# Kernel optimization log

Hardware: AMD Instinct MI355X
Metric: run time of the kernel (lower is better)

## Reference

```python
import jax, jax.numpy as jnp
import numpy as np

J = 1.0          # coupling constant
PT_PERIOD = 4    # parallel-tempering exchange every PT_PERIOD sweeps


def setup_inputs() -> dict:
    key = jax.random.key(0)
    k1, k2 = jax.random.split(key)
    B, C, L = 32, 16, 256
    # temperatures across the Ising critical region, sorted ascending
    T = jnp.sort(1.5 + 2.0 * jax.random.uniform(k1, (B,), dtype=jnp.float32))
    # spins stored as {0,1} ints; converted to +/-1 inside reference
    spins = jax.random.randint(k2, (B, C, L, L), 0, 2).astype(jnp.int32)
    return {"T": T, "spins": spins, "n_sweeps": 16}


def _neighbor_sum(s):
    # periodic 4-neighbor sum, shape preserved [B,C,L,L]
    return (jnp.roll(s, 1, -1) + jnp.roll(s, -1, -1)
            + jnp.roll(s, 1, -2) + jnp.roll(s, -1, -2))


def _energy(s):
    # total Ising energy per chain: -J * sum_<ij> s_i s_j  -> [B, C]
    return -J * jnp.sum(s * (jnp.roll(s, -1, -1) + jnp.roll(s, -1, -2)), axis=(-1, -2))


def reference(T, spins, n_sweeps):
    B, C, L, _ = spins.shape
    s = spins.astype(jnp.float32) * 2.0 - 1.0          # +/-1 spins
    ii = jnp.arange(L)
    parity = (ii[:, None] + ii[None, :]) % 2            # [L,L] checkerboard
    Tb = T[:, None, None, None]                         # [B,1,1,1]
    beta = 1.0 / T                                      # [B]
    base_key = jax.random.key(42)

    def half_sweep(s, key, color):
        dE = 2.0 * J * s * _neighbor_sum(s)             # local energy change on flip
        u = jax.random.uniform(key, s.shape, dtype=jnp.float32)
        acc = u < jnp.exp(-dE / Tb)                     # Metropolis accept
        mask = (parity == color)                        # update one sub-lattice only
        return jnp.where(mask & acc, -s, s)

    def pt_swap(s, key, pair_parity):
        # attempt swaps between adjacent temperatures (b, b+1) with given pair parity
        E = _energy(s)                                  # [B, C]
        d = (beta[:-1] - beta[1:])[:, None] * (E[:-1] - E[1:])   # [B-1, C]
        u = jax.random.uniform(key, (B - 1, C), dtype=jnp.float32)
        pair_mask = (jnp.arange(B - 1) % 2) == pair_parity
        acc = (u < jnp.exp(d)) & pair_mask[:, None]     # [B-1, C] non-overlapping
        swap_next = jnp.concatenate([acc, jnp.zeros((1, C), bool)], 0)  # swap b<->b+1
        swap_prev = jnp.concatenate([jnp.zeros((1, C), bool), acc], 0)
        s_next = jnp.roll(s, -1, axis=0)
        s_prev = jnp.roll(s, 1, axis=0)
        swn = swap_next[:, :, None, None]
        swp = swap_prev[:, :, None, None]
        return jnp.where(swn, s_next, jnp.where(swp, s_prev, s))

    def sweep(s, t):
        kb = jax.random.fold_in(base_key, t)
        k1, k2, k3 = jax.random.split(kb, 3)
        s = half_sweep(s, k1, 0)   # black sub-lattice
        s = half_sweep(s, k2, 1)   # white sub-lattice
        do_pt = (t % PT_PERIOD) == (PT_PERIOD - 1)
        s = jax.lax.cond(do_pt,
                         lambda s_: pt_swap(s_, k3, (t // PT_PERIOD) % 2),
                         lambda s_: s_, s)
        return s, None

    s, _ = jax.lax.scan(sweep, s, jnp.arange(n_sweeps))
    return s, _energy(s)
```

## Files before the change

### kernel.cpp

```cpp
#include <hip/hip_runtime.h>
#include <stdint.h>


#define BB 32
#define CC 16
#define PLANE 65536
#define NSITE (BB * CC * PLANE)
#define NPAIR ((BB - 1) * CC)

__host__ __device__ __forceinline__ void tf2x32(uint32_t k0, uint32_t k1,
                                                uint32_t c0, uint32_t c1,
                                                uint32_t& o0, uint32_t& o1) {
  uint32_t ks2 = k0 ^ k1 ^ 0x1BD11BDAu;
  uint32_t x0 = c0 + k0;
  uint32_t x1 = c1 + k1;
#define TF_ROT(r) { x0 += x1; x1 = (x1 << (r)) | (x1 >> (32 - (r))); x1 ^= x0; }
  TF_ROT(13) TF_ROT(15) TF_ROT(26) TF_ROT(6)
  x0 += k1;  x1 += ks2 + 1u;
  TF_ROT(17) TF_ROT(29) TF_ROT(16) TF_ROT(24)
  x0 += ks2; x1 += k0 + 2u;
  TF_ROT(13) TF_ROT(15) TF_ROT(26) TF_ROT(6)
  x0 += k0;  x1 += k1 + 3u;
  TF_ROT(17) TF_ROT(29) TF_ROT(16) TF_ROT(24)
  x0 += k1;  x1 += ks2 + 4u;
  TF_ROT(13) TF_ROT(15) TF_ROT(26) TF_ROT(6)
  x0 += ks2; x1 += k0 + 5u;
#undef TF_ROT
  o0 = x0; o1 = x1;
}

__device__ __forceinline__ uint32_t tf_bits(uint32_t k0, uint32_t k1,
                                            uint32_t ks2, uint32_t x1i) {
  uint32_t x0 = k0, x1 = x1i;
#define R4(a,b,c,d) \
  x0 += x1; x1 = __builtin_rotateleft32(x1, (a)); x1 ^= x0; \
  x0 += x1; x1 = __builtin_rotateleft32(x1, (b)); x1 ^= x0; \
  x0 += x1; x1 = __builtin_rotateleft32(x1, (c)); x1 ^= x0; \
  x0 += x1; x1 = __builtin_rotateleft32(x1, (d)); x1 ^= x0;
  R4(13,15,26,6)  x0 += k1;  x1 += ks2 + 1u;
  R4(17,29,16,24) x0 += ks2; x1 += k0 + 2u;
  R4(13,15,26,6)  x0 += k0;  x1 += k1 + 3u;
  R4(17,29,16,24) x0 += k1;  x1 += ks2 + 4u;
  R4(13,15,26,6)  x0 += ks2; x1 += k0 + 5u;
#undef R4
  return x0 ^ x1;
}

__device__ __forceinline__ float u01(uint32_t bits) {
  return __uint_as_float((bits >> 9) | 0x3f800000u) - 1.0f;
}

__global__ __launch_bounds__(256) void init8_k(const int* __restrict__ spins,
                                               uint8_t* __restrict__ s) {
  int i = blockIdx.x * 256 + threadIdx.x;
  int4 v = ((const int4*)spins)[i];
  uint32_t o = ((uint32_t)(uint8_t)(int8_t)(2 * v.x - 1))
             | ((uint32_t)(uint8_t)(int8_t)(2 * v.y - 1) << 8)
             | ((uint32_t)(uint8_t)(int8_t)(2 * v.z - 1) << 16)
             | ((uint32_t)(uint8_t)(int8_t)(2 * v.w - 1) << 24);
  ((uint32_t*)s)[i] = o;
}

__global__ void prep_k(const float* __restrict__ T,
                       uint32_t* __restrict__ M4, uint32_t* __restrict__ M8) {
  int b = threadIdx.x;
  if (b < BB) {
    float t = T[b];
    float th4 = (float)exp((double)((-4.0f) / t));
    float th8 = (float)exp((double)((-8.0f) / t));
    M4[b] = (uint32_t)ceil((double)th4 * 8388608.0);
    M8[b] = (uint32_t)ceil((double)th8 * 8388608.0);
  }
}

__device__ __forceinline__ void do_color(uint32_t* __restrict__ tile,
    int w, int lane, int lm, int lp, uint32_t vk, int color,
    uint32_t k0, uint32_t k1, uint32_t ks2, uint32_t M4b, uint32_t M8b) {
#pragma unroll 4
  for (int it = 0; it < 16; ++it) {
    int j  = w + it * 16;
    int rb = j << 6;
    int ju = ((j + 255) & 255) << 6;
    int jd = ((j + 1) & 255) << 6;
    int p  = (j + color) & 1;
    uint32_t soff = (uint32_t)((j << 8) + p);

    uint32_t cur = tile[rb + lane];
    uint32_t up  = tile[ju + lane];
    uint32_t dn  = tile[jd + lane];
    uint32_t pw  = tile[rb + lm];
    uint32_t nw  = tile[rb + lp];
    uint32_t lft = __builtin_amdgcn_alignbit(cur, pw, 24);
    uint32_t rgt = __builtin_amdgcn_alignbit(nw, cur, 8);
    uint32_t kd2 = (up & 0x02020202u) + (dn & 0x02020202u)
                 + (lft & 0x02020202u) + (rgt & 0x02020202u);

    uint32_t flip = 0;
    {
      uint32_t kdi = (kd2 >> (8 * p)) & 0xFFu;
      uint32_t si  = (cur >> (8 * p + 1)) & 1u;
      uint32_t m2  = si ? (8u - kdi) : kdi;
      bool a = true;
      if (m2 < 4u) {
        uint32_t n = tf_bits(k0, k1, ks2, vk + soff) >> 9;
        a = n < (m2 == 2u ? M4b : M8b);
      }
      if (a) flip |= 0xFEu << (8 * p);
    }
    {
      uint32_t kdi = (kd2 >> (8 * p + 16)) & 0xFFu;
      uint32_t si  = (cur >> (8 * p + 17)) & 1u;
      uint32_t m2  = si ? (8u - kdi) : kdi;
      bool a = true;
      if (m2 < 4u) {
        uint32_t n = tf_bits(k0, k1, ks2, vk + soff + 2u) >> 9;
        a = n < (m2 == 2u ? M4b : M8b);
      }
      if (a) flip |= 0xFE0000u << (8 * p);
    }
    tile[rb + lane] = cur ^ flip;
  }
}

__global__ __launch_bounds__(1024) void sweep4_k(
    uint8_t* __restrict__ sg,
    const uint32_t* __restrict__ M4, const uint32_t* __restrict__ M8,
    uint4 kS0, uint4 kS1, uint4 kS2, uint4 kS3,
    int tbase, const int* __restrict__ nsw, float* __restrict__ Eplane) {
  __shared__ uint32_t tile[16384];
  int tid = threadIdx.x;
  int bc  = blockIdx.x;
  int b   = bc >> 4;
  uint32_t bcbase = (uint32_t)bc << 16;
  uint32_t* gp = (uint32_t*)(sg + ((size_t)bc << 16));
  uint32_t M4b = M4[b], M8b = M8[b];
  int nswv = *nsw;

  for (int i = tid; i < 4096; i += 1024)
    ((uint4*)tile)[i] = ((const uint4*)gp)[i];
  __syncthreads();

  int w    = __builtin_amdgcn_readfirstlane(tid >> 6);
  int lane = tid & 63;
  int lm   = (lane + 63) & 63, lp = (lane + 1) & 63;

  uint4 keys[4] = {kS0, kS1, kS2, kS3};
#pragma unroll
  for (int ss = 0; ss < 4; ++ss) {
    if (tbase + ss < nswv) {
      uint32_t kA0 = keys[ss].x, kA1 = keys[ss].y;
      uint32_t kB0 = keys[ss].z, kB1 = keys[ss].w;
      uint32_t ksA = kA0 ^ kA1 ^ 0x1BD11BDAu;
      uint32_t ksB = kB0 ^ kB1 ^ 0x1BD11BDAu;
      uint32_t vkA = kA1 + bcbase + (uint32_t)(lane << 2);
      uint32_t vkB = kB1 + bcbase + (uint32_t)(lane << 2);
      do_color(tile, w, lane, lm, lp, vkA, 0, kA0, kA1, ksA, M4b, M8b);
      __syncthreads();
      do_color(tile, w, lane, lm, lp, vkB, 1, kB0, kB1, ksB, M4b, M8b);
      __syncthreads();
    }
  }

  int acc = 0;
  for (int it = 0; it < 16; ++it) {
    int j = w + it * 16;
    uint32_t cur = tile[(j << 6) + lane];
    uint32_t nxt = tile[(j << 6) + lp];
    uint32_t dwn = tile[((((j + 1) & 255)) << 6) + lane];
    uint32_t rsh = (cur >> 8) | (nxt << 24);
    int d = __builtin_popcount((cur ^ rsh) & 0x02020202u)
          + __builtin_popcount((cur ^ dwn) & 0x02020202u);
    acc += 8 - 2 * d;
  }

  for (int i = tid; i < 4096; i += 1024)
    ((uint4*)gp)[i] = ((uint4*)tile)[i];
  __syncthreads();

  for (int off = 32; off > 0; off >>= 1) acc += __shfl_down(acc, off, 64);
  if (lane == 0) tile[w] = (uint32_t)acc;
  __syncthreads();
  if (tid == 0) {
    int tot = 0;
    for (int i = 0; i < 16; ++i) tot += (int)tile[i];
    Eplane[bc] = -(float)tot;
  }
}

__global__ void pt_decide_k(const float* __restrict__ Eplane,
                            const float* __restrict__ T,
                            uint32_t k0, uint32_t k1, int pair_parity,
                            int* __restrict__ accf, int t,
                            const int* __restrict__ nsw) {
  int tid = threadIdx.x;
  if (tid >= NPAIR) return;
  if (t >= *nsw) { accf[tid] = 0; return; }
  int b = tid >> 4;
  float d = (1.0f / T[b] - 1.0f / T[b + 1]) * (Eplane[tid] - Eplane[tid + 16]);
  uint32_t h0, h1;
  tf2x32(k0, k1, 0u, (uint32_t)tid, h0, h1);
  float u = u01(h0 ^ h1);
  float th = (float)exp((double)d);
  accf[tid] = (u < th) && ((b & 1) == pair_parity);
}

__global__ __launch_bounds__(256) void pt_swap8_k(uint8_t* __restrict__ s,
                                                  const int* __restrict__ accf) {
  int pc = blockIdx.x;
  if (!accf[pc]) return;
  uint4* p0 = (uint4*)(s + ((size_t)pc << 16));
  uint4* p1 = p0 + (CC * PLANE / 16);
  for (int j = threadIdx.x; j < PLANE / 16; j += 256) {
    uint4 a0 = p0[j], a1 = p1[j];
    p0[j] = a1; p1[j] = a0;
  }
}

__global__ void final_eout_k(const float* __restrict__ Eplane,
                             const int* __restrict__ accf,
                             float* __restrict__ Eout) {
  int tid = threadIdx.x;
  int b = tid >> 4;
  float e = Eplane[tid];
  if (b < 31 && accf[tid])      e = Eplane[tid + 16];
  if (b > 0  && accf[tid - 16]) e = Eplane[tid - 16];
  Eout[tid] = e;
}

__global__ __launch_bounds__(256) void expand_k(const int8_t* __restrict__ st,
                                                float* __restrict__ out,
                                                int lo, int cnt4) {
  int i = blockIdx.x * 256 + threadIdx.x;
  if (i >= cnt4) return;
  uint32_t v = *(const uint32_t*)(st + lo + 4 * i);
  float4 o;
  o.x = (float)(int8_t)(v);
  o.y = (float)(int8_t)(v >> 8);
  o.z = (float)(int8_t)(v >> 16);
  o.w = (float)(int8_t)(v >> 24);
  ((float4*)out)[(lo >> 2) + i] = o;
}

__global__ __launch_bounds__(256) void expand_head_k(const int8_t* __restrict__ st,
                                                     float* __restrict__ out) {
  uint32_t r[8];
  int t = threadIdx.x;
  for (int u = 0; u < 8; ++u) r[u] = *(const uint32_t*)(st + t * 32 + 4 * u);
  __syncthreads();
  for (int u = 0; u < 8; ++u) {
    uint32_t v = r[u];
    float4 o;
    o.x = (float)(int8_t)(v);
    o.y = (float)(int8_t)(v >> 8);
    o.z = (float)(int8_t)(v >> 16);
    o.w = (float)(int8_t)(v >> 24);
    ((float4*)out)[t * 8 + u] = o;
  }
}

extern "C" void kernel_launch(void* const* d_in, const int* in_sizes, int n_in,
                              void* d_out, int out_size, void* d_ws, size_t ws_size,
                              hipStream_t stream) {
  (void)in_sizes; (void)n_in; (void)out_size; (void)ws_size;
  const float* T    = (const float*)d_in[0];
  const int*  spins = (const int*)d_in[1];
  const int*  nsw   = (const int*)d_in[2];

  uint8_t* buf0 = (uint8_t*)d_out;
  float*   outf = (float*)d_out;
  float*   Eout = outf + NSITE;

  float*    Eplane = (float*)d_ws;
  uint32_t* M4     = (uint32_t*)(Eplane + 512);
  uint32_t* M8     = M4 + BB;
  int*      accf   = (int*)(M8 + BB);

  init8_k<<<NSITE / 1024, 256, 0, stream>>>(spins, buf0);
  prep_k<<<1, 64, 0, stream>>>(T, M4, M8);

  for (int g = 0; g < 4; ++g) {
    uint4 kS[4];
    uint32_t k3a = 0, k3b = 0;
    for (int i = 0; i < 4; ++i) {
      int t = 4 * g + i;
      uint32_t kb0, kb1;
      tf2x32(0u, 42u, 0u, (uint32_t)t, kb0, kb1);
      tf2x32(kb0, kb1, 0u, 0u, kS[i].x, kS[i].y);
      tf2x32(kb0, kb1, 0u, 1u, kS[i].z, kS[i].w);
      if (i == 3) tf2x32(kb0, kb1, 0u, 2u, k3a, k3b);
    }
    sweep4_k<<<BB * CC, 1024, 0, stream>>>(buf0, M4, M8,
                                           kS[0], kS[1], kS[2], kS[3],
                                           4 * g, nsw, Eplane);
    pt_decide_k<<<1, 512, 0, stream>>>(Eplane, T, k3a, k3b, g & 1,
                                       accf, 4 * g + 3, nsw);
    pt_swap8_k<<<NPAIR, 256, 0, stream>>>(buf0, accf);
  }

  final_eout_k<<<1, 512, 0, stream>>>(Eplane, accf, Eout);

  for (int lo = NSITE / 4; lo >= 8192; lo >>= 2) {
    int cnt4 = (lo * 3) / 4;
    expand_k<<<(cnt4 + 255) / 256, 256, 0, stream>>>((int8_t*)buf0, outf, lo, cnt4);
  }
  expand_head_k<<<1, 256, 0, stream>>>((int8_t*)buf0, outf);
}
```

Before: 1.464 ms.

## Fuse spin init into first sweep kernel and make Metropolis RNG branch-free

Drops the separate init8_k kernel and has the first sweep4_k launch read the int32 spins directly, pack them into int8 in shared memory, and skip one global write-and-read round trip. The Metropolis step now always computes both Threefry draws and picks thresholds with selects, so there is no divergent branch around the RNG. The rotate uses alignbit and the unroll factor drops from 4 to 2. Computing the RNG unconditionally adds ALU work for sites that would have been accepted anyway, in exchange for uniform control flow and less register pressure.

New measurement: 1.731 ms. 1.18x slower.

```diff
diff --git a/kernel.cpp b/kernel.cpp
--- a/kernel.cpp
+++ b/kernel.cpp
@@ -29,36 +29,29 @@
   o0 = x0; o1 = x1;
 }
 
-__device__ __forceinline__ uint32_t tf_bits(uint32_t k0, uint32_t k1,
-                                            uint32_t ks2, uint32_t x1i) {
+__device__ __forceinline__ uint32_t rotl(uint32_t x, int r) {
+  return __builtin_amdgcn_alignbit(x, x, 32 - r);
+}
+
+__device__ __forceinline__ uint32_t tf_bits9(uint32_t k0, uint32_t k1,
+                                             uint32_t ks2, uint32_t x1i) {
   uint32_t x0 = k0, x1 = x1i;
 #define R4(a,b,c,d) \
-  x0 += x1; x1 = __builtin_rotateleft32(x1, (a)); x1 ^= x0; \
-  x0 += x1; x1 = __builtin_rotateleft32(x1, (b)); x1 ^= x0; \
-  x0 += x1; x1 = __builtin_rotateleft32(x1, (c)); x1 ^= x0; \
-  x0 += x1; x1 = __builtin_rotateleft32(x1, (d)); x1 ^= x0;
+  x0 += x1; x1 = rotl(x1, (a)); x1 ^= x0; \
+  x0 += x1; x1 = rotl(x1, (b)); x1 ^= x0; \
+  x0 += x1; x1 = rotl(x1, (c)); x1 ^= x0; \
+  x0 += x1; x1 = rotl(x1, (d)); x1 ^= x0;
   R4(13,15,26,6)  x0 += k1;  x1 += ks2 + 1u;
   R4(17,29,16,24) x0 += ks2; x1 += k0 + 2u;
   R4(13,15,26,6)  x0 += k0;  x1 += k1 + 3u;
   R4(17,29,16,24) x0 += k1;  x1 += ks2 + 4u;
   R4(13,15,26,6)  x0 += ks2; x1 += k0 + 5u;
 #undef R4
-  return x0 ^ x1;
+  return (x0 ^ x1) >> 9;
 }
 
 __device__ __forceinline__ float u01(uint32_t bits) {
   return __uint_as_float((bits >> 9) | 0x3f800000u) - 1.0f;
-}
-
-__global__ __launch_bounds__(256) void init8_k(const int* __restrict__ spins,
-                                               uint8_t* __restrict__ s) {
-  int i = blockIdx.x * 256 + threadIdx.x;
-  int4 v = ((const int4*)spins)[i];
-  uint32_t o = ((uint32_t)(uint8_t)(int8_t)(2 * v.x - 1))
-             | ((uint32_t)(uint8_t)(int8_t)(2 * v.y - 1) << 8)
-             | ((uint32_t)(uint8_t)(int8_t)(2 * v.z - 1) << 16)
-             | ((uint32_t)(uint8_t)(int8_t)(2 * v.w - 1) << 24);
-  ((uint32_t*)s)[i] = o;
 }
 
 __global__ void prep_k(const float* __restrict__ T,
@@ -76,14 +69,14 @@
 __device__ __forceinline__ void do_color(uint32_t* __restrict__ tile,
     int w, int lane, int lm, int lp, uint32_t vk, int color,
     uint32_t k0, uint32_t k1, uint32_t ks2, uint32_t M4b, uint32_t M8b) {
-#pragma unroll 4
+#pragma unroll 2
   for (int it = 0; it < 16; ++it) {
     int j  = w + it * 16;
     int rb = j << 6;
     int ju = ((j + 255) & 255) << 6;
     int jd = ((j + 1) & 255) << 6;
-    int p  = (j + color) & 1;
-    uint32_t soff = (uint32_t)((j << 8) + p);
+    int p8 = ((j + color) & 1) << 3;
+    uint32_t soff = (uint32_t)((j << 8) | (p8 >> 3));
 
     uint32_t cur = tile[rb + lane];
     uint32_t up  = tile[ju + lane];
@@ -95,35 +88,29 @@
     uint32_t kd2 = (up & 0x02020202u) + (dn & 0x02020202u)
                  + (lft & 0x02020202u) + (rgt & 0x02020202u);
 
-    uint32_t flip = 0;
-    {
-      uint32_t kdi = (kd2 >> (8 * p)) & 0xFFu;
-      uint32_t si  = (cur >> (8 * p + 1)) & 1u;
-      uint32_t m2  = si ? (8u - kdi) : kdi;
-      bool a = true;
-      if (m2 < 4u) {
-        uint32_t n = tf_bits(k0, k1, ks2, vk + soff) >> 9;
-        a = n < (m2 == 2u ? M4b : M8b);
-      }
-      if (a) flip |= 0xFEu << (8 * p);
-    }
-    {
-      uint32_t kdi = (kd2 >> (8 * p + 16)) & 0xFFu;
-      uint32_t si  = (cur >> (8 * p + 17)) & 1u;
-      uint32_t m2  = si ? (8u - kdi) : kdi;
-      bool a = true;
-      if (m2 < 4u) {
-        uint32_t n = tf_bits(k0, k1, ks2, vk + soff + 2u) >> 9;
-        a = n < (m2 == 2u ? M4b : M8b);
-      }
-      if (a) flip |= 0xFE0000u << (8 * p);
-    }
+    uint32_t nA = tf_bits9(k0, k1, ks2, vk + soff);
+    uint32_t nB = tf_bits9(k0, k1, ks2, vk + soff + 2u);
+
+    uint32_t kdA = (kd2 >> p8) & 0xFFu;
+    uint32_t sA  = (cur >> (p8 + 1)) & 1u;
+    uint32_t m2A = sA ? (8u - kdA) : kdA;
+    uint32_t thA = (m2A == 2u) ? M4b : M8b;
+    if (m2A >= 4u) thA = 0xFFFFFFFFu;
+    uint32_t flip = (nA < thA) ? (0xFEu << p8) : 0u;
+
+    uint32_t kdB = (kd2 >> (p8 + 16)) & 0xFFu;
+    uint32_t sB  = (cur >> (p8 + 17)) & 1u;
+    uint32_t m2B = sB ? (8u - kdB) : kdB;
+    uint32_t thB = (m2B == 2u) ? M4b : M8b;
+    if (m2B >= 4u) thB = 0xFFFFFFFFu;
+    if (nB < thB) flip |= (0xFE0000u << p8);
+
     tile[rb + lane] = cur ^ flip;
   }
 }
 
 __global__ __launch_bounds__(1024) void sweep4_k(
-    uint8_t* __restrict__ sg,
+    uint8_t* __restrict__ sg, const int* __restrict__ spins, int doInit,
     const uint32_t* __restrict__ M4, const uint32_t* __restrict__ M8,
     uint4 kS0, uint4 kS1, uint4 kS2, uint4 kS3,
     int tbase, const int* __restrict__ nsw, float* __restrict__ Eplane) {
@@ -136,8 +123,19 @@
   uint32_t M4b = M4[b], M8b = M8[b];
   int nswv = *nsw;
 
-  for (int i = tid; i < 4096; i += 1024)
-    ((uint4*)tile)[i] = ((const uint4*)gp)[i];
+  if (doInit) {
+    const int4* ip = (const int4*)(spins + ((size_t)bc << 16));
+    for (int i = tid; i < 16384; i += 1024) {
+      int4 v = ip[i];
+      tile[i] = ((uint32_t)(uint8_t)(int8_t)(2 * v.x - 1))
+              | ((uint32_t)(uint8_t)(int8_t)(2 * v.y - 1) << 8)
+              | ((uint32_t)(uint8_t)(int8_t)(2 * v.z - 1) << 16)
+              | ((uint32_t)(uint8_t)(int8_t)(2 * v.w - 1) << 24);
+    }
+  } else {
+    for (int i = tid; i < 4096; i += 1024)
+      ((uint4*)tile)[i] = ((const uint4*)gp)[i];
+  }
   __syncthreads();
 
   int w    = __builtin_amdgcn_readfirstlane(tid >> 6);
@@ -275,7 +273,6 @@
   uint32_t* M8     = M4 + BB;
   int*      accf   = (int*)(M8 + BB);
 
-  init8_k<<<NSITE / 1024, 256, 0, stream>>>(spins, buf0);
   prep_k<<<1, 64, 0, stream>>>(T, M4, M8);
 
   for (int g = 0; g < 4; ++g) {
@@ -289,7 +286,8 @@
       tf2x32(kb0, kb1, 0u, 1u, kS[i].z, kS[i].w);
       if (i == 3) tf2x32(kb0, kb1, 0u, 2u, k3a, k3b);
     }
-    sweep4_k<<<BB * CC, 1024, 0, stream>>>(buf0, M4, M8,
+    sweep4_k<<<BB * CC, 1024, 0, stream>>>(buf0, spins, (g == 0) ? 1 : 0,
+                                           M4, M8,
                                            kS[0], kS[1], kS[2], kS[3],
                                            4 * g, nsw, Eplane);
     pt_decide_k<<<1, 512, 0, stream>>>(Eplane, T, k3a, k3b, g & 1,
```

## Fuse PT decision into swap kernels and permute final state into workspace

Applied to the files above, without the earlier changes.

Drops the separate pt_decide kernel: each swap block now computes its own pair's acceptance inline. The prep kernel is merged into init. For the final exchange, when the workspace is large enough, the state is copied with the swap permutation applied into a workspace buffer and then expanded in one pass. This replaces the in-place swap plus the multi-launch backward expand chain and removes several kernel launches. The Threefry rotate is also switched to alignbit.

New measurement: 1.454 ms. No clear change (-0.7%).

```diff
diff --git a/kernel.cpp b/kernel.cpp
--- a/kernel.cpp
+++ b/kernel.cpp
@@ -29,14 +29,18 @@
   o0 = x0; o1 = x1;
 }
 
+__device__ __forceinline__ uint32_t rotl(uint32_t x, int r) {
+  return __builtin_amdgcn_alignbit(x, x, 32 - r);
+}
+
 __device__ __forceinline__ uint32_t tf_bits(uint32_t k0, uint32_t k1,
                                             uint32_t ks2, uint32_t x1i) {
   uint32_t x0 = k0, x1 = x1i;
 #define R4(a,b,c,d) \
-  x0 += x1; x1 = __builtin_rotateleft32(x1, (a)); x1 ^= x0; \
-  x0 += x1; x1 = __builtin_rotateleft32(x1, (b)); x1 ^= x0; \
-  x0 += x1; x1 = __builtin_rotateleft32(x1, (c)); x1 ^= x0; \
-  x0 += x1; x1 = __builtin_rotateleft32(x1, (d)); x1 ^= x0;
+  x0 += x1; x1 = rotl(x1, (a)); x1 ^= x0; \
+  x0 += x1; x1 = rotl(x1, (b)); x1 ^= x0; \
+  x0 += x1; x1 = rotl(x1, (c)); x1 ^= x0; \
+  x0 += x1; x1 = rotl(x1, (d)); x1 ^= x0;
   R4(13,15,26,6)  x0 += k1;  x1 += ks2 + 1u;
   R4(17,29,16,24) x0 += ks2; x1 += k0 + 2u;
   R4(13,15,26,6)  x0 += k0;  x1 += k1 + 3u;
@@ -50,8 +54,23 @@
   return __uint_as_float((bits >> 9) | 0x3f800000u) - 1.0f;
 }
 
-__global__ __launch_bounds__(256) void init8_k(const int* __restrict__ spins,
-                                               uint8_t* __restrict__ s) {
+__device__ __forceinline__ bool pt_accept(int pair, const float* Eplane,
+                                          const float* T,
+                                          uint32_t k0, uint32_t k1) {
+  int b = pair >> 4;
+  float d = (1.0f / T[b] - 1.0f / T[b + 1])
+          * (Eplane[pair] - Eplane[pair + 16]);
+  uint32_t h0, h1;
+  tf2x32(k0, k1, 0u, (uint32_t)pair, h0, h1);
+  float u = u01(h0 ^ h1);
+  float th = (float)exp((double)d);
+  return u < th;
+}
+
+__global__ __launch_bounds__(256) void init8_prep_k(
+    const int* __restrict__ spins, uint8_t* __restrict__ s,
+    const float* __restrict__ T,
+    uint32_t* __restrict__ M4, uint32_t* __restrict__ M8) {
   int i = blockIdx.x * 256 + threadIdx.x;
   int4 v = ((const int4*)spins)[i];
   uint32_t o = ((uint32_t)(uint8_t)(int8_t)(2 * v.x - 1))
@@ -59,12 +78,8 @@
              | ((uint32_t)(uint8_t)(int8_t)(2 * v.z - 1) << 16)
              | ((uint32_t)(uint8_t)(int8_t)(2 * v.w - 1) << 24);
   ((uint32_t*)s)[i] = o;
-}
-
-__global__ void prep_k(const float* __restrict__ T,
-                       uint32_t* __restrict__ M4, uint32_t* __restrict__ M8) {
-  int b = threadIdx.x;
-  if (b < BB) {
+  if (blockIdx.x == 0 && threadIdx.x < BB) {
+    int b = threadIdx.x;
     float t = T[b];
     float th4 = (float)exp((double)((-4.0f) / t));
     float th8 = (float)exp((double)((-8.0f) / t));
@@ -187,27 +202,15 @@
   }
 }
 
-__global__ void pt_decide_k(const float* __restrict__ Eplane,
-                            const float* __restrict__ T,
-                            uint32_t k0, uint32_t k1, int pair_parity,
-                            int* __restrict__ accf, int t,
-                            const int* __restrict__ nsw) {
-  int tid = threadIdx.x;
-  if (tid >= NPAIR) return;
-  if (t >= *nsw) { accf[tid] = 0; return; }
-  int b = tid >> 4;
-  float d = (1.0f / T[b] - 1.0f / T[b + 1]) * (Eplane[tid] - Eplane[tid + 16]);
-  uint32_t h0, h1;
-  tf2x32(k0, k1, 0u, (uint32_t)tid, h0, h1);
-  float u = u01(h0 ^ h1);
-  float th = (float)exp((double)d);
-  accf[tid] = (u < th) && ((b & 1) == pair_parity);
-}
-
-__global__ __launch_bounds__(256) void pt_swap8_k(uint8_t* __restrict__ s,
-                                                  const int* __restrict__ accf) {
+__global__ __launch_bounds__(256) void pt_swapD_k(uint8_t* __restrict__ s,
+    const float* __restrict__ Eplane, const float* __restrict__ T,
+    uint32_t k0, uint32_t k1, int pair_parity, int t,
+    const int* __restrict__ nsw) {
   int pc = blockIdx.x;
-  if (!accf[pc]) return;
+  int b  = pc >> 4;
+  if ((b & 1) != pair_parity) return;
+  if (t >= *nsw) return;
+  if (!pt_accept(pc, Eplane, T, k0, k1)) return;
   uint4* p0 = (uint4*)(s + ((size_t)pc << 16));
   uint4* p1 = p0 + (CC * PLANE / 16);
   for (int j = threadIdx.x; j < PLANE / 16; j += 256) {
@@ -216,15 +219,54 @@
   }
 }
 
-__global__ void final_eout_k(const float* __restrict__ Eplane,
-                             const int* __restrict__ accf,
-                             float* __restrict__ Eout) {
-  int tid = threadIdx.x;
-  int b = tid >> 4;
-  float e = Eplane[tid];
-  if (b < 31 && accf[tid])      e = Eplane[tid + 16];
-  if (b > 0  && accf[tid - 16]) e = Eplane[tid - 16];
-  Eout[tid] = e;
+__device__ __forceinline__ int perm_src(int pc, const float* Eplane,
+                                        const float* T, uint32_t k0,
+                                        uint32_t k1, int pair_parity,
+                                        int t, int nswv) {
+  int b = pc >> 4;
+  if (t < nswv) {
+    if (b < 31 && (b & 1) == pair_parity &&
+        pt_accept(pc, Eplane, T, k0, k1)) return pc + 16;
+    if (b > 0 && ((b - 1) & 1) == pair_parity &&
+        pt_accept(pc - 16, Eplane, T, k0, k1)) return pc - 16;
+  }
+  return pc;
+}
+
+__global__ __launch_bounds__(256) void permute_out_k(
+    const uint8_t* __restrict__ s, uint8_t* __restrict__ dst,
+    const float* __restrict__ Eplane, const float* __restrict__ T,
+    uint32_t k0, uint32_t k1, int pair_parity, int t,
+    const int* __restrict__ nsw, float* __restrict__ Eout) {
+  int pc = blockIdx.x;
+  int src = perm_src(pc, Eplane, T, k0, k1, pair_parity, t, *nsw);
+  const uint4* p0 = (const uint4*)(s + ((size_t)src << 16));
+  uint4*       p1 = (uint4*)(dst + ((size_t)pc << 16));
+  for (int j = threadIdx.x; j < PLANE / 16; j += 256)
+    p1[j] = p0[j];
+  if (threadIdx.x == 0) Eout[pc] = Eplane[src];
+}
+
+__global__ __launch_bounds__(256) void expand_full_k(
+    const uint8_t* __restrict__ st, float* __restrict__ out) {
+  int i = blockIdx.x * 256 + threadIdx.x;
+  uint32_t v = ((const uint32_t*)st)[i];
+  float4 o;
+  o.x = (float)(int8_t)(v);
+  o.y = (float)(int8_t)(v >> 8);
+  o.z = (float)(int8_t)(v >> 16);
+  o.w = (float)(int8_t)(v >> 24);
+  ((float4*)out)[i] = o;
+}
+
+__global__ void final_eoutD_k(const float* __restrict__ Eplane,
+                              const float* __restrict__ T,
+                              uint32_t k0, uint32_t k1, int pair_parity,
+                              int t, const int* __restrict__ nsw,
+                              float* __restrict__ Eout) {
+  int pc = threadIdx.x;
+  int src = perm_src(pc, Eplane, T, k0, k1, pair_parity, t, *nsw);
+  Eout[pc] = Eplane[src];
 }
 
 __global__ __launch_bounds__(256) void expand_k(const int8_t* __restrict__ st,
@@ -261,7 +303,7 @@
 extern "C" void kernel_launch(void* const* d_in, const int* in_sizes, int n_in,
                               void* d_out, int out_size, void* d_ws, size_t ws_size,
                               hipStream_t stream) {
-  (void)in_sizes; (void)n_in; (void)out_size; (void)ws_size;
+  (void)in_sizes; (void)n_in; (void)out_size;
   const float* T    = (const float*)d_in[0];
   const int*  spins = (const int*)d_in[1];
   const int*  nsw   = (const int*)d_in[2];
@@ -273,11 +315,12 @@
   float*    Eplane = (float*)d_ws;
   uint32_t* M4     = (uint32_t*)(Eplane + 512);
   uint32_t* M8     = M4 + BB;
-  int*      accf   = (int*)(M8 + BB);
-
-  init8_k<<<NSITE / 1024, 256, 0, stream>>>(spins, buf0);
-  prep_k<<<1, 64, 0, stream>>>(T, M4, M8);
-
+  uint8_t*  wstate = (uint8_t*)d_ws + 4096;
+  bool big_ws = (ws_size >= (size_t)NSITE + 4096);
+
+  init8_prep_k<<<NSITE / 1024, 256, 0, stream>>>(spins, buf0, T, M4, M8);
+
+  uint32_t k3fa = 0, k3fb = 0;
   for (int g = 0; g < 4; ++g) {
     uint4 kS[4];
     uint32_t k3a = 0, k3b = 0;
@@ -292,16 +335,28 @@
     sweep4_k<<<BB * CC, 1024, 0, stream>>>(buf0, M4, M8,
                                            kS[0], kS[1], kS[2], kS[3],
                                            4 * g, nsw, Eplane);
-    pt_decide_k<<<1, 512, 0, stream>>>(Eplane, T, k3a, k3b, g & 1,
-                                       accf, 4 * g + 3, nsw);
-    pt_swap8_k<<<NPAIR, 256, 0, stream>>>(buf0, accf);
-  }
-
-  final_eout_k<<<1, 512, 0, stream>>>(Eplane, accf, Eout);
-
-  for (int lo = NSITE / 4; lo >= 8192; lo >>= 2) {
-    int cnt4 = (lo * 3) / 4;
-    expand_k<<<(cnt4 + 255) / 256, 256, 0, stream>>>((int8_t*)buf0, outf, lo, cnt4);
-  }
-  expand_head_k<<<1, 256, 0, stream>>>((int8_t*)buf0, outf);
-}
+    if (g < 3) {
+      pt_swapD_k<<<NPAIR, 256, 0, stream>>>(buf0, Eplane, T, k3a, k3b,
+                                            g & 1, 4 * g + 3, nsw);
+    } else {
+      k3fa = k3a; k3fb = k3b;
+    }
+  }
+
+  if (big_ws) {
+    permute_out_k<<<BB * CC, 256, 0, stream>>>(buf0, wstate, Eplane, T,
+                                               k3fa, k3fb, 1, 15, nsw, Eout);
+    expand_full_k<<<NSITE / 1024, 256, 0, stream>>>(wstate, outf);
+  } else {
+    pt_swapD_k<<<NPAIR, 256, 0, stream>>>(buf0, Eplane, T, k3fa, k3fb,
+                                          1, 15, nsw);
+    final_eoutD_k<<<1, 512, 0, stream>>>(Eplane, T, k3fa, k3fb, 1, 15,
+                                         nsw, Eout);
+    for (int lo = NSITE / 4; lo >= 8192; lo >>= 2) {
+      int cnt4 = (lo * 3) / 4;
+      expand_k<<<(cnt4 + 255) / 256, 256, 0, stream>>>((int8_t*)buf0, outf,
+                                                       lo, cnt4);
+    }
+    expand_head_k<<<1, 256, 0, stream>>>((int8_t*)buf0, outf);
+  }
+}
```
